# Performance work log

Hardware: AMD Instinct MI355X
Metric: run time of the kernel (lower is better)

Reference implementation:

```python
import jax, jax.numpy as jnp
import numpy as np

_BIG = 1e4  # kornia uses 1e4 as the 'infinity' for masked-out kernel positions


def _windows(img, pad_val):
    """Return the 9 shifted 3x3 neighborhoods of img, stacked on axis 0.
    img: [B,C,H,W] -> [9,B,C,H,W]. Border padded with pad_val so padded
    pixels never win the min (erosion) / max (dilation), matching kornia.
    """
    B, C, H, W = img.shape
    p = jnp.pad(img, ((0, 0), (0, 0), (1, 1), (1, 1)), constant_values=pad_val)
    return jnp.stack([p[..., i:i + H, j:j + W]
                      for i in range(3) for j in range(3)], axis=0)


def _erosion(img, mask):
    w = _windows(img, _BIG)
    return jnp.min(jnp.where(mask, w, _BIG), axis=0)


def _dilation(img, mask):
    w = _windows(img, -_BIG)
    return jnp.max(jnp.where(mask, w, -_BIG), axis=0)


def setup_inputs() -> dict:
    key = jax.random.key(0)
    img = jax.random.uniform(key, (8, 3, 1024, 1024), dtype=jnp.float32)
    # kernel0: symmetric 3x3 cross structuring element
    kernel = jnp.array([[0, 1, 0], [1, 1, 1], [0, 1, 0]], dtype=jnp.int32)
    return {"img": img, "kernel": kernel}


def reference(img, kernel):
    # morphological opening = erosion followed by dilation, same structuring element
    mask = (kernel.reshape(9, 1, 1, 1, 1) == 1)
    eroded = _erosion(img, mask)
    opened = _dilation(eroded, mask)
    return opened
```

## Files before the change

### kernel.cpp

```cpp
#include <hip/hip_runtime.h>

#define BIGV 1e4f

constexpr int TW = 128;
constexpr int TH = 16;

__global__ __launch_bounds__(256) void opening_kernel(
    const float* __restrict__ img, const int* __restrict__ kern,
    float* __restrict__ out, int H, int W)
{
    __shared__ float s_img[TH + 4][TW + 4];
    __shared__ float s_ero[TH + 2][TW + 2];

    const int tid   = threadIdx.x;
    const int x0    = blockIdx.x * TW;
    const int y0    = blockIdx.y * TH;
    const size_t pbase = (size_t)blockIdx.z * H * W;

    bool m[9];
#pragma unroll
    for (int k = 0; k < 9; ++k) m[k] = (kern[k] == 1);

    for (int idx = tid; idx < (TH + 4) * (TW + 4); idx += 256) {
        int r  = idx / (TW + 4);
        int c  = idx % (TW + 4);
        int gy = y0 - 2 + r;
        int gx = x0 - 2 + c;
        float v = BIGV;
        if (gy >= 0 && gy < H && gx >= 0 && gx < W)
            v = img[pbase + (size_t)gy * W + gx];
        s_img[r][c] = v;
    }
    __syncthreads();

    for (int idx = tid; idx < (TH + 2) * (TW + 2); idx += 256) {
        int r  = idx / (TW + 2);
        int c  = idx % (TW + 2);
        int gy = y0 - 1 + r;
        int gx = x0 - 1 + c;
        float e = -BIGV;
        if (gy >= 0 && gy < H && gx >= 0 && gx < W) {
            e = BIGV;
#pragma unroll
            for (int k = 0; k < 9; ++k) {
                const int di = k / 3, dj = k % 3;
                float v = s_img[r + di][c + dj];
                e = fminf(e, m[k] ? v : BIGV);
            }
        }
        s_ero[r][c] = e;
    }
    __syncthreads();

    for (int idx = tid; idx < TH * TW; idx += 256) {
        int r = idx >> 7;
        int c = idx & (TW - 1);
        float d = -BIGV;
#pragma unroll
        for (int k = 0; k < 9; ++k) {
            const int di = k / 3, dj = k % 3;
            float v = s_ero[r + di][c + dj];
            d = fmaxf(d, m[k] ? v : -BIGV);
        }
        int gy = y0 + r, gx = x0 + c;
        if (gy < H && gx < W)
            out[pbase + (size_t)gy * W + gx] = d;
    }
}

extern "C" void kernel_launch(void* const* d_in, const int* in_sizes, int n_in,
                              void* d_out, int out_size, void* d_ws, size_t ws_size,
                              hipStream_t stream) {
    const float* img  = (const float*)d_in[0];
    const int*   kern = (const int*)d_in[1];
    float*       out  = (float*)d_out;

    const int H = 1024, W = 1024;
    const int planes = in_sizes[0] / (H * W);

    dim3 block(256);
    dim3 grid((W + TW - 1) / TW, (H + TH - 1) / TH, planes);
    opening_kernel<<<grid, block, 0, stream>>>(img, kern, out, H, W);
}
```

Measured before the change: 213.5 us.

## Replace shared-memory tiling with register-streaming rows and cross-kernel fast path

The shared-memory two-stage tile kernel is replaced by a register-resident sliding window. Each thread handles 8 contiguous pixels and streams down 8 rows, using vectorized float4/float2 loads, prefetching the next row, and writing with nontemporal vector stores. A specialized path for the cross structuring element cuts the masked 9-tap min/max to 5 taps. This removes LDS traffic and block barriers, at the cost of redundant halo row loads per thread strip and an assumption that W and H divide the tile sizes.

```diff
diff --git a/kernel.cpp b/kernel.cpp
--- a/kernel.cpp
+++ b/kernel.cpp
@@ -2,70 +2,172 @@
 
 #define BIGV 1e4f
 
-constexpr int TW = 128;
-constexpr int TH = 16;
+constexpr int RH = 8;
+constexpr int TY = 4;
+constexpr int PX = 8;
+
+typedef float nf4 __attribute__((ext_vector_type(4)));
+
+struct Raw { float4 m0, m1; float2 L, R; };
+struct Ero { float e[10]; };
+
+__device__ __forceinline__ float min3f(float a, float b, float c) { return fminf(fminf(a, b), c); }
+__device__ __forceinline__ float max3f(float a, float b, float c) { return fmaxf(fmaxf(a, b), c); }
+
+__device__ __forceinline__ float rv(const Raw& r, int i) {
+    switch (i) {
+        case 0:  return r.L.x;  case 1:  return r.L.y;
+        case 2:  return r.m0.x; case 3:  return r.m0.y;
+        case 4:  return r.m0.z; case 5:  return r.m0.w;
+        case 6:  return r.m1.x; case 7:  return r.m1.y;
+        case 8:  return r.m1.z; case 9:  return r.m1.w;
+        case 10: return r.R.x;  default: return r.R.y;
+    }
+}
+
+__device__ __forceinline__ Raw load_raw(const float* __restrict__ img, int y, int x,
+                                        int H, int W) {
+    Raw r;
+    if (y >= 0 && y < H) {
+        const float* q = img + (size_t)y * W;
+        r.m0 = *(const float4*)(q + x);
+        r.m1 = *(const float4*)(q + x + 4);
+        r.L = make_float2(BIGV, BIGV);
+        r.R = make_float2(BIGV, BIGV);
+        if (x > 0)      r.L = *(const float2*)(q + x - 2);
+        if (x + PX < W) r.R = *(const float2*)(q + x + PX);
+    } else {
+        r.m0 = make_float4(BIGV, BIGV, BIGV, BIGV);
+        r.m1 = r.m0;
+        r.L = make_float2(BIGV, BIGV);
+        r.R = r.L;
+    }
+    return r;
+}
+
+__device__ __forceinline__ Ero erode_cross(const Raw& a, const Raw& b, const Raw& c,
+                                           int y, int H, int x, int W) {
+    Ero e;
+    if (y >= 0 && y < H) {
+#pragma unroll
+        for (int j = 0; j < 10; ++j) {
+            float v = min3f(rv(a, j + 1), rv(b, j + 1), rv(c, j + 1));
+            e.e[j] = min3f(v, rv(b, j), rv(b, j + 2));
+        }
+        if (x == 0)      e.e[0] = -BIGV;
+        if (x + PX >= W) e.e[9] = -BIGV;
+    } else {
+#pragma unroll
+        for (int j = 0; j < 10; ++j) e.e[j] = -BIGV;
+    }
+    return e;
+}
+
+__device__ __forceinline__ void dilate_cross(const Ero& t, const Ero& m, const Ero& b,
+                                             nf4& o0, nf4& o1) {
+    float o[PX];
+#pragma unroll
+    for (int j = 0; j < PX; ++j)
+        o[j] = max3f(max3f(t.e[j + 1], m.e[j + 1], b.e[j + 1]), m.e[j], m.e[j + 2]);
+    o0 = (nf4){o[0], o[1], o[2], o[3]};
+    o1 = (nf4){o[4], o[5], o[6], o[7]};
+}
+
+__device__ __forceinline__ Ero erode_gen(const Raw& a, const Raw& b, const Raw& c,
+                                         const bool* m, int y, int H, int x, int W) {
+    Ero e;
+    if (y >= 0 && y < H) {
+#pragma unroll
+        for (int j = 0; j < 10; ++j) {
+            float acc = BIGV;
+#pragma unroll
+            for (int k = 0; k < 9; ++k) {
+                const int di = k / 3, dj = k % 3;
+                const Raw& rr = (di == 0) ? a : ((di == 1) ? b : c);
+                acc = fminf(acc, m[k] ? rv(rr, j + dj) : BIGV);
+            }
+            e.e[j] = acc;
+        }
+        if (x == 0)      e.e[0] = -BIGV;
+        if (x + PX >= W) e.e[9] = -BIGV;
+    } else {
+#pragma unroll
+        for (int j = 0; j < 10; ++j) e.e[j] = -BIGV;
+    }
+    return e;
+}
+
+__device__ __forceinline__ void dilate_gen(const Ero& t, const Ero& md, const Ero& b,
+                                           const bool* m, nf4& o0, nf4& o1) {
+    float o[PX];
+#pragma unroll
+    for (int j = 0; j < PX; ++j) {
+        float acc = -BIGV;
+#pragma unroll
+        for (int k = 0; k < 9; ++k) {
+            const int di = k / 3, dj = k % 3;
+            const Ero& ee = (di == 0) ? t : ((di == 1) ? md : b);
+            acc = fmaxf(acc, m[k] ? ee.e[j + dj] : -BIGV);
+        }
+        o[j] = acc;
+    }
+    o0 = (nf4){o[0], o[1], o[2], o[3]};
+    o1 = (nf4){o[4], o[5], o[6], o[7]};
+}
+
+template <bool CROSS>
+__device__ __forceinline__ void run(const float* __restrict__ img, float* __restrict__ out,
+                                    const bool* m, int x, int y0, int H, int W) {
+    Raw r0 = load_raw(img, y0 - 2, x, H, W);
+    Raw r1 = load_raw(img, y0 - 1, x, H, W);
+    Raw r2 = load_raw(img, y0,     x, H, W);
+    Raw r3 = load_raw(img, y0 + 1, x, H, W);
+    Raw pf = load_raw(img, y0 + 2, x, H, W);
+
+    Ero E0 = CROSS ? erode_cross(r0, r1, r2, y0 - 1, H, x, W)
+                   : erode_gen(r0, r1, r2, m, y0 - 1, H, x, W);
+    Ero E1 = CROSS ? erode_cross(r1, r2, r3, y0, H, x, W)
+                   : erode_gen(r1, r2, r3, m, y0, H, x, W);
+    Raw A = r2, B = r3;
+
+#pragma unroll
+    for (int i = 0; i < RH; ++i) {
+        const int y = y0 + i;
+        Raw nf = pf;
+        if (i < RH - 1)
+            nf = load_raw(img, y + 3, x, H, W);
+        Ero E2 = CROSS ? erode_cross(A, B, pf, y + 1, H, x, W)
+                       : erode_gen(A, B, pf, m, y + 1, H, x, W);
+        nf4 o0, o1;
+        if (CROSS) dilate_cross(E0, E1, E2, o0, o1);
+        else       dilate_gen(E0, E1, E2, m, o0, o1);
+        float* po = out + (size_t)y * W + x;
+        __builtin_nontemporal_store(o0, (nf4*)po);
+        __builtin_nontemporal_store(o1, (nf4*)(po + 4));
+        A = B; B = pf; pf = nf;
+        E0 = E1; E1 = E2;
+    }
+}
 
 __global__ __launch_bounds__(256) void opening_kernel(
     const float* __restrict__ img, const int* __restrict__ kern,
     float* __restrict__ out, int H, int W)
 {
-    __shared__ float s_img[TH + 4][TW + 4];
-    __shared__ float s_ero[TH + 2][TW + 2];
-
-    const int tid   = threadIdx.x;
-    const int x0    = blockIdx.x * TW;
-    const int y0    = blockIdx.y * TH;
+    const int lx = threadIdx.x & 63;
+    const int ty = threadIdx.x >> 6;
+    const int x  = blockIdx.x * (64 * PX) + lx * PX;
+    const int y0 = (blockIdx.y * TY + ty) * RH;
     const size_t pbase = (size_t)blockIdx.z * H * W;
 
     bool m[9];
 #pragma unroll
     for (int k = 0; k < 9; ++k) m[k] = (kern[k] == 1);
 
-    for (int idx = tid; idx < (TH + 4) * (TW + 4); idx += 256) {
-        int r  = idx / (TW + 4);
-        int c  = idx % (TW + 4);
-        int gy = y0 - 2 + r;
-        int gx = x0 - 2 + c;
-        float v = BIGV;
-        if (gy >= 0 && gy < H && gx >= 0 && gx < W)
-            v = img[pbase + (size_t)gy * W + gx];
-        s_img[r][c] = v;
-    }
-    __syncthreads();
+    const bool cross = m[1] && m[3] && m[4] && m[5] && m[7] &&
+                       !m[0] && !m[2] && !m[6] && !m[8];
 
-    for (int idx = tid; idx < (TH + 2) * (TW + 2); idx += 256) {
-        int r  = idx / (TW + 2);
-        int c  = idx % (TW + 2);
-        int gy = y0 - 1 + r;
-        int gx = x0 - 1 + c;
-        float e = -BIGV;
-        if (gy >= 0 && gy < H && gx >= 0 && gx < W) {
-            e = BIGV;
-#pragma unroll
-            for (int k = 0; k < 9; ++k) {
-                const int di = k / 3, dj = k % 3;
-                float v = s_img[r + di][c + dj];
-                e = fminf(e, m[k] ? v : BIGV);
-            }
-        }
-        s_ero[r][c] = e;
-    }
-    __syncthreads();
-
-    for (int idx = tid; idx < TH * TW; idx += 256) {
-        int r = idx >> 7;
-        int c = idx & (TW - 1);
-        float d = -BIGV;
-#pragma unroll
-        for (int k = 0; k < 9; ++k) {
-            const int di = k / 3, dj = k % 3;
-            float v = s_ero[r + di][c + dj];
-            d = fmaxf(d, m[k] ? v : -BIGV);
-        }
-        int gy = y0 + r, gx = x0 + c;
-        if (gy < H && gx < W)
-            out[pbase + (size_t)gy * W + gx] = d;
-    }
+    if (cross) run<true >(img + pbase, out + pbase, m, x, y0, H, W);
+    else       run<false>(img + pbase, out + pbase, m, x, y0, H, W);
 }
 
 extern "C" void kernel_launch(void* const* d_in, const int* in_sizes, int n_in,
@@ -79,6 +181,6 @@
     const int planes = in_sizes[0] / (H * W);
 
     dim3 block(256);
-    dim3 grid((W + TW - 1) / TW, (H + TH - 1) / TH, planes);
+    dim3 grid(W / (64 * PX), H / (TY * RH), planes);
     opening_kernel<<<grid, block, 0, stream>>>(img, kern, out, H, W);
 }
```

After: 187.8 us. -12.0%, faster.
